# Kernel optimization log

Measured on AMD Instinct MI355X. Metric: run time of the kernel, lower is better.

Reference implementation:

```python
import jax, jax.numpy as jnp
import numpy as np

N_SAMPLES = 2 ** 15          # 32768
STEP = 256                   # transform_step_size
WIN = 2048                   # transform/synthesis window
N_FRAMES = N_SAMPLES // STEP # 128
N_COEFFS = WIN // 2 + 1      # 1025
DILATIONS = (1, 2, 4, 8, 16, 32, 64, 1)


def hann(n):
    return 0.5 - 0.5 * jnp.cos(2.0 * jnp.pi * jnp.arange(n, dtype=jnp.float32) / n)


def transform(audio):
    # audio: (B, 1, N) -> magnitude STFT (B, 1024, 128)
    x = audio[:, 0, :]
    x = jnp.pad(x, ((0, 0), (0, WIN - STEP)))  # pad so n_frames == N_SAMPLES // STEP
    idx = np.arange(N_FRAMES)[:, None] * STEP + np.arange(WIN)[None, :]
    frames = x[:, idx] * hann(WIN)
    spec = jnp.abs(jnp.fft.rfft(frames, norm='ortho'))   # (B, F, 1025)
    return spec[..., : N_COEFFS - 1].transpose(0, 2, 1)  # (B, 1024, F)


def conv1x1(x, w, b):
    # x: (B, I, T), w: (O, I, 1), b: (O,)
    return jnp.einsum('oi,bit->bot', w[:, :, 0], x) + b[None, :, None]


def anticausal_block(x, w, b, dilation):
    # kernel_size=2 anti-causal dilated conv: looks at t and t+dilation (pad future)
    x_fut = jnp.pad(x, ((0, 0), (0, 0), (0, dilation)))[:, :, dilation:]
    y = (jnp.einsum('oi,bit->bot', w[:, :, 0], x)
         + jnp.einsum('oi,bit->bot', w[:, :, 1], x_fut)
         + b[None, :, None])
    y = jax.nn.leaky_relu(y, 0.2)
    y = y + x
    # do_norm: per-example max-norm
    y = y / (jnp.max(jnp.abs(y), axis=(1, 2), keepdims=True) + 1e-8)
    return y


def upsample_with_holes(x, desired_size):
    # zero-stuffing upsample: out[..., ::step] = x
    b, c, t = x.shape
    step = desired_size // t
    out = jnp.zeros((b, c, desired_size), x.dtype)
    return out.at[:, :, ::step].set(x)


def freq_domain_resonance(coeffs):
    # coeffs: (1, C, 1025) in [0, 1); per-frame decay = repeated spectral multiply
    c = jnp.clip(coeffs, 0.0, 0.9999)
    exps = jnp.arange(1, N_FRAMES + 1, dtype=coeffs.dtype)
    mags = c[:, :, None, :] ** exps[None, None, :, None]     # (1, C, F, 1025)
    frames = jnp.fft.irfft(mags, n=WIN) * hann(WIN)
    hop = WIN // 2
    total = hop * (N_FRAMES - 1) + WIN
    idx = np.arange(N_FRAMES)[:, None] * hop + np.arange(WIN)[None, :]
    out = jnp.zeros(frames.shape[:2] + (total,), frames.dtype)
    out = out.at[:, :, idx].add(frames)                      # overlap-add
    return out[..., :N_SAMPLES]                              # (1, C, N)


def fft_convolve(a, b):
    # circular-free conv via zero-padding to 2N, keep first N (matches repo fft_convolve)
    n = a.shape[-1]
    spec = jnp.fft.rfft(a, n=2 * n) * jnp.fft.rfft(b, n=2 * n)
    return jnp.fft.irfft(spec, n=2 * n)[..., :n]


def reference(audio, proj_in_w, proj_in_b, blocks_w, blocks_b,
              proj_sparse_w, proj_sparse_b, proj_dense_w, proj_dense_b, resonances):
    spec = transform(audio)                         # (B, 1024, 128)
    h = conv1x1(spec, proj_in_w, proj_in_b)         # (B, 32, 128)
    acc = jnp.zeros_like(h)
    for i, d in enumerate(DILATIONS):               # fixed 8-block stack
        h = anticausal_block(h, blocks_w[i], blocks_b[i], d)
        acc = acc + h
    x = conv1x1(acc, proj_sparse_w, proj_sparse_b)  # (B, 256, 128)
    sparse = jax.nn.relu(x)
    x = conv1x1(sparse, proj_dense_w, proj_dense_b) # (B, 32, 128)
    x = upsample_with_holes(x, N_SAMPLES)           # (B, 32, 32768)
    res = freq_domain_resonance(resonances)         # (1, 32, 32768), broadcast over B
    y = fft_convolve(x, res)                        # (B, 32, 32768)
    y = jnp.sum(y, axis=1, keepdims=True)           # (B, 1, 32768)
    return y, sparse


def setup_inputs() -> dict:
    key = jax.random.key(0)
    ks = jax.random.split(key, 12)
    u = lambda k, shape: jax.random.uniform(k, shape, jnp.float32, -0.05, 0.05)
    return {
        'audio': jax.random.normal(ks[0], (32, 1, N_SAMPLES), jnp.float32),
        'proj_in_w': u(ks[1], (32, 1024, 1)),
        'proj_in_b': jnp.zeros((32,), jnp.float32),
        'blocks_w': u(ks[2], (8, 32, 32, 2)),
        'blocks_b': jnp.zeros((8, 32), jnp.float32),
        'proj_sparse_w': u(ks[3], (256, 32, 1)),
        'proj_sparse_b': jnp.zeros((256,), jnp.float32),
        'proj_dense_w': u(ks[4], (32, 256, 1)),
        'proj_dense_b': jnp.zeros((32,), jnp.float32),
        'resonances': jax.random.uniform(ks[5], (1, 32, N_COEFFS), jnp.float32, 0.0, 1.0),
    }
```

## Files before the change

### kernel.cpp

```cpp
#include <hip/hip_runtime.h>

#define PI_F 3.14159265358979323846f

typedef short bf16x8 __attribute__((ext_vector_type(8)));
typedef float f32x4 __attribute__((ext_vector_type(4)));

#define MFMA16(acc, a, b) \
  acc = __builtin_amdgcn_mfma_f32_16x16x32_bf16(a, b, acc, 0, 0, 0)

#define WS_SPEC   0u
#define WS_H0     4194304u
#define WS_ACC    4325376u
#define WS_V      4456448u
#define WS_WTIN   4587520u
#define WS_WST    4620288u
#define WS_WDT    4628480u
#define WS_FRAMES 4636672u
#define WS_RES    6733824u

__device__ __forceinline__ void fft2048_stages(float2* buf, int tid) {
  for (int stage = 0; stage < 11; ++stage) {
    int half = 1 << stage;
    float base = -PI_F / (float)half;
    for (int t = tid; t < 1024; t += 256) {
      int j  = t & (half - 1);
      int i0 = ((t >> stage) << (stage + 1)) + j;
      int i1 = i0 + half;
      float s, c;
      __sincosf(base * (float)j, &s, &c);
      float2 u = buf[i0];
      float2 w = buf[i1];
      float tr = c * w.x - s * w.y;
      float ti = c * w.y + s * w.x;
      buf[i0] = make_float2(u.x + tr, u.y + ti);
      buf[i1] = make_float2(u.x - tr, u.y - ti);
    }
    __syncthreads();
  }
}

__global__ __launch_bounds__(256) void k_fft(const float* __restrict__ audio,
                                             const float* __restrict__ resin,
                                             float* __restrict__ spec,
                                             float* __restrict__ frames) {
  __shared__ float2 buf[2048];
  int blk = blockIdx.x;
  if (blk < 2048) {
    int b  = blk >> 6;
    int f0 = (blk & 63) * 2;
    for (int j = threadIdx.x; j < 2048; j += 256) {
      float h = 0.5f - 0.5f * __cosf(0.0030679615757712823f * (float)j);
      int i1 = f0 * 256 + j;
      int i2 = i1 + 256;
      float a1 = (i1 < 32768) ? audio[b * 32768 + i1] : 0.f;
      float a2 = (i2 < 32768) ? audio[b * 32768 + i2] : 0.f;
      buf[__brev((unsigned)j) >> 21] = make_float2(a1 * h, a2 * h);
    }
    __syncthreads();
    fft2048_stages(buf, threadIdx.x);
    const float scale = 0.5f * 0.022097086912079608f;
    for (int k = threadIdx.x; k < 1024; k += 256) {
      float2 zk = buf[k];
      float2 zn = buf[(2048 - k) & 2047];
      float f1r = zk.x + zn.x, f1i = zk.y - zn.y;
      float f2r = zk.y + zn.y, f2i = zk.x - zn.x;
      spec[(b * 128 + f0) * 1024 + k]     = sqrtf(f1r * f1r + f1i * f1i) * scale;
      spec[(b * 128 + f0 + 1) * 1024 + k] = sqrtf(f2r * f2r + f2i * f2i) * scale;
    }
  } else {
    int r = blk - 2048;
    int c = r >> 4;
    int g = r & 15;
    float e1 = (float)(2 * g + 1);
    for (int k = threadIdx.x; k < 2048; k += 256) {
      int kk = (k <= 1024) ? k : 2048 - k;
      float cv = resin[c * 1025 + kk];
      cv = fminf(fmaxf(cv, 0.f), 0.9999f);
      float m1 = __powf(cv, e1);
      float m2 = m1 * cv;
      buf[__brev((unsigned)k) >> 21] = make_float2(m1, m2);
    }
    __syncthreads();
    fft2048_stages(buf, threadIdx.x);
    for (int j = threadIdx.x; j < 2048; j += 256) {
      float h  = 0.5f - 0.5f * __cosf(0.0030679615757712823f * (float)j);
      float sc = h * (1.f / 2048.f);
      float2 z = buf[j];
      frames[(c * 32 + 2 * g) * 2048 + j]     = z.x * sc;
      frames[(c * 32 + 2 * g + 1) * 2048 + j] = z.y * sc;
    }
  }
}

__global__ __launch_bounds__(256) void k_prep(const float* __restrict__ Win,
                                              const float* __restrict__ Ws,
                                              const float* __restrict__ Wd,
                                              const float* __restrict__ bwIn,
                                              float* __restrict__ WT,
                                              float* __restrict__ WsT,
                                              float* __restrict__ WdT,
                                              short* __restrict__ Whg,
                                              short* __restrict__ Wlg) {
  int i = blockIdx.x * 256 + threadIdx.x;
  if (i < 32768) { int o = i >> 10, k = i & 1023; WT[k * 32 + o] = Win[i]; }
  if (i < 8192)  { int o2 = i >> 5, m = i & 31;   WsT[m * 256 + o2] = Ws[i]; }
  if (i < 8192)  { int c = i >> 8, o2 = i & 255;  WdT[o2 * 32 + c] = Wd[i]; }
  if (i < 16384) {
    int w = i & 1, m = (i >> 1) & 31, o = (i >> 6) & 31, s = i >> 11;
    float val = bwIn[i];
    unsigned bits = __float_as_uint(val);
    float rem = val - __uint_as_float(bits & 0xffff0000u);
    int row = (s * 2 + w) * 32 + o;
    Whg[row * 32 + m] = (short)(bits >> 16);
    Wlg[row * 32 + m] = (short)(__float_as_uint(rem) >> 16);
  }
}

__global__ __launch_bounds__(256) void k_proj_in(const float* __restrict__ spec,
                                                 const float* __restrict__ WT,
                                                 const float* __restrict__ bias,
                                                 float* __restrict__ h0) {
  __shared__ float specL[8][1024];
  __shared__ float red[32][8][8];
  int b  = blockIdx.x >> 4;
  int t0 = (blockIdx.x & 15) * 8;
  for (int i = threadIdx.x; i < 8192; i += 256) {
    int tt = i >> 10, k = i & 1023;
    specL[tt][k] = spec[(b * 128 + t0 + tt) * 1024 + k];
  }
  __syncthreads();
  int o = threadIdx.x & 31, p = threadIdx.x >> 5;
  float part[8] = {0.f,0.f,0.f,0.f,0.f,0.f,0.f,0.f};
  for (int i = 0; i < 128; ++i) {
    int k = p * 128 + ((i + p * 4) & 127);
    float w = WT[k * 32 + o];
#pragma unroll
    for (int tt = 0; tt < 8; ++tt) part[tt] += w * specL[tt][k];
  }
#pragma unroll
  for (int tt = 0; tt < 8; ++tt) red[o][tt][p] = part[tt];
  __syncthreads();
  int oo = threadIdx.x >> 3, tt2 = threadIdx.x & 7;
  float s = bias[oo];
#pragma unroll
  for (int p2 = 0; p2 < 8; ++p2) s += red[oo][tt2][p2];
  h0[b * 4096 + oo * 128 + t0 + tt2] = s;
}

__global__ __launch_bounds__(1024) void k_chain(const float* __restrict__ h0,
                                                const short* __restrict__ Whg,
                                                const short* __restrict__ Wlg,
                                                const float* __restrict__ bb,
                                                float* __restrict__ accout) {
  __shared__ __align__(16) short Hh[192 * 40];
  __shared__ __align__(16) short Hl[192 * 40];
  __shared__ float Hf[128 * 33];
  __shared__ float bL[256];
  __shared__ float red[16];
  int b = blockIdx.x, tid = threadIdx.x;

  for (int i = tid; i < 4096; i += 1024) {
    int t = i & 127;
    int o = i >> 7;
    float val = h0[b * 4096 + i];
    Hf[t * 33 + o] = val;
    unsigned bits = __float_as_uint(val);
    float rem = val - __uint_as_float(bits & 0xffff0000u);
    Hh[t * 40 + o] = (short)(bits >> 16);
    Hl[t * 40 + o] = (short)(__float_as_uint(rem) >> 16);
  }
  for (int i = tid; i < 64 * 40; i += 1024) {
    Hh[128 * 40 + i] = 0;
    Hl[128 * 40 + i] = 0;
  }
  if (tid < 256) bL[tid] = bb[tid];
  __syncthreads();

  int wave = tid >> 6, lane = tid & 63;
  int quad = lane >> 4, l15 = lane & 15;
  int t0 = (wave & 7) * 16, o0 = (wave >> 3) * 16;
  int tD = t0 + quad * 4;
  int oD = o0 + l15;

  const bf16x8* Hh8 = (const bf16x8*)Hh;
  const bf16x8* Hl8 = (const bf16x8*)Hl;
  const bf16x8* Wh8 = (const bf16x8*)Whg;
  const bf16x8* Wl8 = (const bf16x8*)Wlg;

  float accsum[4] = {0.f, 0.f, 0.f, 0.f};
  const int DIL[8] = {1, 2, 4, 8, 16, 32, 64, 1};

#pragma unroll
  for (int s = 0; s < 8; ++s) {
    int arow = t0 + l15;
    int frow = arow + DIL[s];
    bf16x8 Ah = Hh8[arow * 5 + quad];
    bf16x8 Al = Hl8[arow * 5 + quad];
    bf16x8 Fh = Hh8[frow * 5 + quad];
    bf16x8 Fl = Hl8[frow * 5 + quad];
    int w0row = ((s * 2 + 0) * 32 + oD) * 4 + quad;
    int w1row = ((s * 2 + 1) * 32 + oD) * 4 + quad;
    bf16x8 B0h = Wh8[w0row], B0l = Wl8[w0row];
    bf16x8 B1h = Wh8[w1row], B1l = Wl8[w1row];
    float bias = bL[s * 32 + oD];
    f32x4 acc = {bias, bias, bias, bias};
    MFMA16(acc, Ah, B0h); MFMA16(acc, Ah, B0l); MFMA16(acc, Al, B0h);
    MFMA16(acc, Fh, B1h); MFMA16(acc, Fh, B1l); MFMA16(acc, Fl, B1h);
    float hnew[4], lmax = 0.f;
#pragma unroll
    for (int r = 0; r < 4; ++r) {
      float sv = acc[r];
      sv = (sv > 0.f) ? sv : 0.2f * sv;
      sv += Hf[(tD + r) * 33 + oD];
      hnew[r] = sv;
      lmax = fmaxf(lmax, fabsf(sv));
    }
#pragma unroll
    for (int off = 32; off > 0; off >>= 1)
      lmax = fmaxf(lmax, __shfl_down(lmax, off, 64));
    if (lane == 0) red[wave] = lmax;
    __syncthreads();
    float mx = red[0];
#pragma unroll
    for (int i = 1; i < 16; ++i) mx = fmaxf(mx, red[i]);
    float nm = 1.f / (mx + 1e-8f);
#pragma unroll
    for (int r = 0; r < 4; ++r) {
      float hv = hnew[r] * nm;
      accsum[r] += hv;
      int t = tD + r;
      Hf[t * 33 + oD] = hv;
      unsigned bits = __float_as_uint(hv);
      float rem = hv - __uint_as_float(bits & 0xffff0000u);
      Hh[t * 40 + oD] = (short)(bits >> 16);
      Hl[t * 40 + oD] = (short)(__float_as_uint(rem) >> 16);
    }
    __syncthreads();
  }
#pragma unroll
  for (int r = 0; r < 4; ++r)
    accout[b * 4096 + (tD + r) * 32 + oD] = accsum[r];
}

__global__ __launch_bounds__(256) void k_sparse_dense(const float* __restrict__ acc,
                                                      const float* __restrict__ WsT,
                                                      const float* __restrict__ bs,
                                                      const float* __restrict__ WdT,
                                                      const float* __restrict__ bd,
                                                      float* __restrict__ out_sparse,
                                                      float* __restrict__ v) {
  __shared__ float accL[32];
  __shared__ float sL[256];
  __shared__ float red[8][32];
  int b = blockIdx.x >> 7, t = blockIdx.x & 127;
  int tid = threadIdx.x;
  if (tid < 32) accL[tid] = acc[b * 4096 + t * 32 + tid];
  __syncthreads();
  float s = bs[tid];
  for (int m = 0; m < 32; ++m) s += WsT[m * 256 + tid] * accL[m];
  s = fmaxf(s, 0.f);
  out_sparse[b * 32768 + tid * 128 + t] = s;
  sL[tid] = s;
  __syncthreads();
  int c = tid & 31, p = tid >> 5;
  float part = 0.f;
  for (int j = 0; j < 32; ++j) {
    int o2 = p * 32 + j;
    part += WdT[o2 * 32 + c] * sL[o2];
  }
  red[p][c] = part;
  __syncthreads();
  if (tid < 32) {
    float vv = bd[tid];
    for (int p2 = 0; p2 < 8; ++p2) vv += red[p2][tid];
    v[b * 4096 + tid * 128 + t] = vv;
  }
}

__global__ __launch_bounds__(256) void k_res_assemble(const float* __restrict__ frames,
                                                      float* __restrict__ res) {
  int i = blockIdx.x * 256 + threadIdx.x;
  int c = i >> 15, s = i & 32767;
  int g = s >> 10, j0 = s & 1023;
  float v = frames[(c * 32 + g) * 2048 + j0];
  if (g > 0) v += frames[(c * 32 + g - 1) * 2048 + j0 + 1024];
  res[i] = v;
}

__global__ __launch_bounds__(256) void k_bpack(const float* __restrict__ res,
                                               short* __restrict__ Bh,
                                               short* __restrict__ Bl) {
  int c = blockIdx.x >> 4, o = blockIdx.x & 15;
  int r = threadIdx.x;
  bf16x8 hv, lv;
#pragma unroll
  for (int j = 0; j < 8; ++j) {
    float val = res[c * 32768 + (8 * o + j) * 256 + r];
    unsigned bits = __float_as_uint(val);
    float rem = val - __uint_as_float(bits & 0xffff0000u);
    hv[j] = (short)(bits >> 16);
    lv[j] = (short)(__float_as_uint(rem) >> 16);
  }
  int unit = (blockIdx.x * 16 + (r >> 4)) * 16 + (r & 15);
  ((bf16x8*)Bh)[unit] = hv;
  ((bf16x8*)Bl)[unit] = lv;
}

__global__ __launch_bounds__(256) void k_conv(const float* __restrict__ v,
                                              const short* __restrict__ Bh,
                                              const short* __restrict__ Bl,
                                              float* __restrict__ y) {
  __shared__ float vwin[32][33];
  __shared__ __align__(16) short Ah[16 * 520];
  __shared__ __align__(16) short Al[16 * 520];
  int blk = blockIdx.x;
  int b = blk / 36;
  int p = blk - b * 36;
  int qt = (int)((sqrtf(8.f * (float)p + 1.f) - 1.f) * 0.5f + 1e-4f);
  int uc = p - ((qt * (qt + 1)) >> 1);
  int q0 = qt * 16, u0 = uc * 16;
  int D0 = q0 - u0;

  for (int i = threadIdx.x; i < 1024; i += 256) {
    int c = i >> 5, ii = i & 31;
    int d = D0 - 15 + ii;
    vwin[c][ii] = (d >= 0 && d < 128) ? v[b * 4096 + c * 128 + d] : 0.f;
  }
  __syncthreads();
  for (int idx = threadIdx.x; idx < 8192; idx += 256) {
    int m = idx >> 9, kk = idx & 511;
    float val = vwin[kk >> 4][(m - (kk & 15)) + 15];
    unsigned bits = __float_as_uint(val);
    float rem = val - __uint_as_float(bits & 0xffff0000u);
    Ah[m * 520 + kk] = (short)(bits >> 16);
    Al[m * 520 + kk] = (short)(__float_as_uint(rem) >> 16);
  }
  __syncthreads();

  int lane = threadIdx.x & 63, wave = threadIdx.x >> 6;
  int quad = lane >> 4, l15 = lane & 15;
  int nt0 = wave * 4;

  f32x4 acc[4];
#pragma unroll
  for (int i = 0; i < 4; ++i) acc[i] = (f32x4)0.f;

  const bf16x8* Ah8 = (const bf16x8*)Ah;
  const bf16x8* Al8 = (const bf16x8*)Al;
  const bf16x8* Bh8 = (const bf16x8*)Bh;
  const bf16x8* Bl8 = (const bf16x8*)Bl;
  int aoff = l15 * 65 + quad;
  int og   = 2 * uc + (quad & 1);
  int cq   = quad >> 1;

#pragma unroll
  for (int ks = 0; ks < 16; ++ks) {
    bf16x8 avh = Ah8[aoff + 4 * ks];
    bf16x8 avl = Al8[aoff + 4 * ks];
    int c = 2 * ks + cq;
    int bbase = (c * 16 + og) * 256 + l15;
#pragma unroll
    for (int t = 0; t < 4; ++t) {
      int bi = bbase + (nt0 + t) * 16;
      bf16x8 bvh = Bh8[bi];
      bf16x8 bvl = Bl8[bi];
      MFMA16(acc[t], avh, bvh);
      MFMA16(acc[t], avh, bvl);
      MFMA16(acc[t], avl, bvh);
    }
  }

  float* yb = y + b * 32768 + (q0 + quad * 4) * 256 + l15;
#pragma unroll
  for (int t = 0; t < 4; ++t)
#pragma unroll
    for (int reg = 0; reg < 4; ++reg)
      atomicAdd(yb + reg * 256 + (nt0 + t) * 16, acc[t][reg]);
}

extern "C" void kernel_launch(void* const* d_in, const int* in_sizes, int n_in,
                              void* d_out, int out_size, void* d_ws, size_t ws_size,
                              hipStream_t stream) {
  const float* audio = (const float*)d_in[0];
  const float* Win   = (const float*)d_in[1];
  const float* bin   = (const float*)d_in[2];
  const float* bw    = (const float*)d_in[3];
  const float* bb    = (const float*)d_in[4];
  const float* Ws    = (const float*)d_in[5];
  const float* bs    = (const float*)d_in[6];
  const float* Wd    = (const float*)d_in[7];
  const float* bd    = (const float*)d_in[8];
  const float* reson = (const float*)d_in[9];

  float* out = (float*)d_out;
  float* ws  = (float*)d_ws;

  float* spec   = ws + WS_SPEC;
  float* h0     = ws + WS_H0;
  float* accb   = ws + WS_ACC;
  float* vbuf   = ws + WS_V;
  float* WT     = ws + WS_WTIN;
  float* WsT    = ws + WS_WST;
  float* WdT    = ws + WS_WDT;
  float* frames = ws + WS_FRAMES;
  float* resbuf = ws + WS_RES;
  short* Bh = (short*)(ws + WS_FRAMES);
  short* Bl = (short*)(ws + WS_FRAMES + 524288u);
  short* Whg = (short*)(ws + WS_V);
  short* Wlg = (short*)(ws + WS_V + 8192u);

  hipMemsetAsync(d_out, 0, 1048576u * sizeof(float), stream);

  k_prep<<<128, 256, 0, stream>>>(Win, Ws, Wd, bw, WT, WsT, WdT, Whg, Wlg);
  k_fft<<<2560, 256, 0, stream>>>(audio, reson, spec, frames);
  k_res_assemble<<<4096, 256, 0, stream>>>(frames, resbuf);
  k_bpack<<<512, 256, 0, stream>>>(resbuf, Bh, Bl);
  k_proj_in<<<512, 256, 0, stream>>>(spec, WT, bin, h0);
  k_chain<<<32, 1024, 0, stream>>>(h0, Whg, Wlg, bb, accb);
  k_sparse_dense<<<4096, 256, 0, stream>>>(accb, WsT, bs, WdT, bd, out + 1048576, vbuf);
  k_conv<<<1152, 256, 0, stream>>>(vbuf, Bh, Bl, out);
}
```

Baseline: 209.8 us.

## Prepack Toeplitz A operand globally and reuse B fragments across four output tiles

```diff
diff --git a/kernel.cpp b/kernel.cpp
--- a/kernel.cpp
+++ b/kernel.cpp
@@ -306,76 +306,85 @@
   ((bf16x8*)Bl)[unit] = lv;
 }
 
-__global__ __launch_bounds__(256) void k_conv(const float* __restrict__ v,
+__global__ __launch_bounds__(256) void k_apack(const float* __restrict__ v,
+                                               short* __restrict__ Ahx,
+                                               short* __restrict__ Alx) {
+  int row = blockIdx.x;
+  int b = row >> 7, mp = row & 127;
+  for (int kk = threadIdx.x; kk < 512; kk += 256) {
+    int c = kk >> 4, u = kk & 15, d = mp - u;
+    float val = (d >= 0) ? v[b * 4096 + c * 128 + d] : 0.f;
+    unsigned bits = __float_as_uint(val);
+    float rem = val - __uint_as_float(bits & 0xffff0000u);
+    Ahx[row * 512 + kk] = (short)(bits >> 16);
+    Alx[row * 512 + kk] = (short)(__float_as_uint(rem) >> 16);
+  }
+}
+
+__global__ __launch_bounds__(256) void k_conv(const short* __restrict__ Ahx,
+                                              const short* __restrict__ Alx,
                                               const short* __restrict__ Bh,
                                               const short* __restrict__ Bl,
                                               float* __restrict__ y) {
-  __shared__ float vwin[32][33];
-  __shared__ __align__(16) short Ah[16 * 520];
-  __shared__ __align__(16) short Al[16 * 520];
+  const int UC[12]  = {0,0,1,1,2,2,3,3,4,5,6,7};
+  const int QT0[12] = {0,4,1,5,2,6,3,7,4,5,6,7};
+  const int QN[12]  = {4,4,4,3,4,2,4,1,4,3,2,1};
   int blk = blockIdx.x;
-  int b = blk / 36;
-  int p = blk - b * 36;
-  int qt = (int)((sqrtf(8.f * (float)p + 1.f) - 1.f) * 0.5f + 1e-4f);
-  int uc = p - ((qt * (qt + 1)) >> 1);
-  int q0 = qt * 16, u0 = uc * 16;
-  int D0 = q0 - u0;
-
-  for (int i = threadIdx.x; i < 1024; i += 256) {
-    int c = i >> 5, ii = i & 31;
-    int d = D0 - 15 + ii;
-    vwin[c][ii] = (d >= 0 && d < 128) ? v[b * 4096 + c * 128 + d] : 0.f;
-  }
-  __syncthreads();
-  for (int idx = threadIdx.x; idx < 8192; idx += 256) {
-    int m = idx >> 9, kk = idx & 511;
-    float val = vwin[kk >> 4][(m - (kk & 15)) + 15];
-    unsigned bits = __float_as_uint(val);
-    float rem = val - __uint_as_float(bits & 0xffff0000u);
-    Ah[m * 520 + kk] = (short)(bits >> 16);
-    Al[m * 520 + kk] = (short)(__float_as_uint(rem) >> 16);
-  }
-  __syncthreads();
-
+  int b = blk / 12, g = blk - b * 12;
+  int uc = UC[g], qt0v = QT0[g], qn = QN[g];
   int lane = threadIdx.x & 63, wave = threadIdx.x >> 6;
   int quad = lane >> 4, l15 = lane & 15;
   int nt0 = wave * 4;
-
-  f32x4 acc[4];
-#pragma unroll
-  for (int i = 0; i < 4; ++i) acc[i] = (f32x4)0.f;
-
-  const bf16x8* Ah8 = (const bf16x8*)Ah;
-  const bf16x8* Al8 = (const bf16x8*)Al;
+  int og = 2 * uc + (quad & 1);
+  int cq = quad >> 1;
+
+  f32x4 acc[4][4];
+#pragma unroll
+  for (int j = 0; j < 4; ++j)
+#pragma unroll
+    for (int t = 0; t < 4; ++t) acc[j][t] = (f32x4)0.f;
+
+  const bf16x8* Ah8 = (const bf16x8*)Ahx;
+  const bf16x8* Al8 = (const bf16x8*)Alx;
   const bf16x8* Bh8 = (const bf16x8*)Bh;
   const bf16x8* Bl8 = (const bf16x8*)Bl;
-  int aoff = l15 * 65 + quad;
-  int og   = 2 * uc + (quad & 1);
-  int cq   = quad >> 1;
+  int abase0 = (b * 128 + (qt0v - uc) * 16 + l15) * 64 + quad;
 
 #pragma unroll
   for (int ks = 0; ks < 16; ++ks) {
-    bf16x8 avh = Ah8[aoff + 4 * ks];
-    bf16x8 avl = Al8[aoff + 4 * ks];
     int c = 2 * ks + cq;
     int bbase = (c * 16 + og) * 256 + l15;
+    bf16x8 bvh[4], bvl[4];
 #pragma unroll
     for (int t = 0; t < 4; ++t) {
       int bi = bbase + (nt0 + t) * 16;
-      bf16x8 bvh = Bh8[bi];
-      bf16x8 bvl = Bl8[bi];
-      MFMA16(acc[t], avh, bvh);
-      MFMA16(acc[t], avh, bvl);
-      MFMA16(acc[t], avl, bvh);
-    }
-  }
-
-  float* yb = y + b * 32768 + (q0 + quad * 4) * 256 + l15;
-#pragma unroll
-  for (int t = 0; t < 4; ++t)
-#pragma unroll
-    for (int reg = 0; reg < 4; ++reg)
-      atomicAdd(yb + reg * 256 + (nt0 + t) * 16, acc[t][reg]);
+      bvh[t] = Bh8[bi];
+      bvl[t] = Bl8[bi];
+    }
+#pragma unroll
+    for (int j = 0; j < 4; ++j) {
+      int ai = abase0 + j * 1024 + 4 * ks;
+      bf16x8 avh = Ah8[ai];
+      bf16x8 avl = Al8[ai];
+#pragma unroll
+      for (int t = 0; t < 4; ++t) {
+        MFMA16(acc[j][t], avh, bvh[t]);
+        MFMA16(acc[j][t], avh, bvl[t]);
+        MFMA16(acc[j][t], avl, bvh[t]);
+      }
+    }
+  }
+
+#pragma unroll
+  for (int j = 0; j < 4; ++j) {
+    if (j >= qn) break;
+    float* yb = y + b * 32768 + ((qt0v + j) * 16 + quad * 4) * 256 + l15;
+#pragma unroll
+    for (int t = 0; t < 4; ++t)
+#pragma unroll
+      for (int reg = 0; reg < 4; ++reg)
+        atomicAdd(yb + reg * 256 + (nt0 + t) * 16, acc[j][t][reg]);
+  }
 }
 
 extern "C" void kernel_launch(void* const* d_in, const int* in_sizes, int n_in,
@@ -408,6 +417,8 @@
   short* Bl = (short*)(ws + WS_FRAMES + 524288u);
   short* Whg = (short*)(ws + WS_V);
   short* Wlg = (short*)(ws + WS_V + 8192u);
+  short* Ahx = (short*)(ws + WS_SPEC);
+  short* Alx = (short*)(ws + WS_SPEC + 1048576u);
 
   hipMemsetAsync(d_out, 0, 1048576u * sizeof(float), stream);
 
@@ -418,5 +429,6 @@
   k_proj_in<<<512, 256, 0, stream>>>(spec, WT, bin, h0);
   k_chain<<<32, 1024, 0, stream>>>(h0, Whg, Wlg, bb, accb);
   k_sparse_dense<<<4096, 256, 0, stream>>>(accb, WsT, bs, WdT, bd, out + 1048576, vbuf);
-  k_conv<<<1152, 256, 0, stream>>>(vbuf, Bh, Bl, out);
-}
+  k_apack<<<4096, 256, 0, stream>>>(vbuf, Ahx, Alx);
+  k_conv<<<384, 256, 0, stream>>>(Ahx, Alx, Bh, Bl, out);
+}
```

Measured after the change: 225.0 us. 1.07x slower.

## Replace Toeplitz MFMA convolution with polyphase FFT convolution over frame index

Applied to the files above, without the earlier changes.

```diff
diff --git a/kernel.cpp b/kernel.cpp
--- a/kernel.cpp
+++ b/kernel.cpp
@@ -8,6 +8,11 @@
 #define MFMA16(acc, a, b) \
   acc = __builtin_amdgcn_mfma_f32_16x16x32_bf16(a, b, acc, 0, 0, 0)
 
+#define WS_RR     0u
+#define WS_RI     1056768u
+#define WS_VR     2113536u
+#define WS_VI     2245632u
+#define WS_YR     2377728u
 #define WS_SPEC   0u
 #define WS_H0     4194304u
 #define WS_ACC    4325376u
@@ -16,7 +21,7 @@
 #define WS_WST    4620288u
 #define WS_WDT    4628480u
 #define WS_FRAMES 4636672u
-#define WS_RES    6733824u
+#define WS_YI     4636672u
 
 __device__ __forceinline__ void fft2048_stages(float2* buf, int tid) {
   for (int stage = 0; stage < 11; ++stage) {
@@ -34,6 +39,29 @@
       float ti = c * w.y + s * w.x;
       buf[i0] = make_float2(u.x + tr, u.y + ti);
       buf[i1] = make_float2(u.x - tr, u.y - ti);
+    }
+    __syncthreads();
+  }
+}
+
+template<int NROWS>
+__device__ __forceinline__ void fft256_rows(float2 (*buf)[256], int tid, float sgn) {
+  for (int stage = 0; stage < 8; ++stage) {
+    int half = 1 << stage;
+    float base = sgn * PI_F / (float)half;
+    for (int t = tid; t < NROWS * 128; t += 256) {
+      int row = t >> 7, tt = t & 127;
+      int j  = tt & (half - 1);
+      int i0 = ((tt >> stage) << (stage + 1)) + j;
+      int i1 = i0 + half;
+      float s, c;
+      __sincosf(base * (float)j, &s, &c);
+      float2 u = buf[row][i0];
+      float2 w = buf[row][i1];
+      float tr = c * w.x - s * w.y;
+      float ti = c * w.y + s * w.x;
+      buf[row][i0] = make_float2(u.x + tr, u.y + ti);
+      buf[row][i1] = make_float2(u.x - tr, u.y - ti);
     }
     __syncthreads();
   }
@@ -277,105 +305,113 @@
   }
 }
 
-__global__ __launch_bounds__(256) void k_res_assemble(const float* __restrict__ frames,
-                                                      float* __restrict__ res) {
-  int i = blockIdx.x * 256 + threadIdx.x;
-  int c = i >> 15, s = i & 32767;
-  int g = s >> 10, j0 = s & 1023;
-  float v = frames[(c * 32 + g) * 2048 + j0];
-  if (g > 0) v += frames[(c * 32 + g - 1) * 2048 + j0 + 1024];
-  res[i] = v;
-}
-
-__global__ __launch_bounds__(256) void k_bpack(const float* __restrict__ res,
-                                               short* __restrict__ Bh,
-                                               short* __restrict__ Bl) {
-  int c = blockIdx.x >> 4, o = blockIdx.x & 15;
-  int r = threadIdx.x;
-  bf16x8 hv, lv;
-#pragma unroll
-  for (int j = 0; j < 8; ++j) {
-    float val = res[c * 32768 + (8 * o + j) * 256 + r];
-    unsigned bits = __float_as_uint(val);
-    float rem = val - __uint_as_float(bits & 0xffff0000u);
-    hv[j] = (short)(bits >> 16);
-    lv[j] = (short)(__float_as_uint(rem) >> 16);
-  }
-  int unit = (blockIdx.x * 16 + (r >> 4)) * 16 + (r & 15);
-  ((bf16x8*)Bh)[unit] = hv;
-  ((bf16x8*)Bl)[unit] = lv;
-}
-
-__global__ __launch_bounds__(256) void k_conv(const float* __restrict__ v,
-                                              const short* __restrict__ Bh,
-                                              const short* __restrict__ Bl,
-                                              float* __restrict__ y) {
-  __shared__ float vwin[32][33];
-  __shared__ __align__(16) short Ah[16 * 520];
-  __shared__ __align__(16) short Al[16 * 520];
-  int blk = blockIdx.x;
-  int b = blk / 36;
-  int p = blk - b * 36;
-  int qt = (int)((sqrtf(8.f * (float)p + 1.f) - 1.f) * 0.5f + 1e-4f);
-  int uc = p - ((qt * (qt + 1)) >> 1);
-  int q0 = qt * 16, u0 = uc * 16;
-  int D0 = q0 - u0;
-
-  for (int i = threadIdx.x; i < 1024; i += 256) {
-    int c = i >> 5, ii = i & 31;
-    int d = D0 - 15 + ii;
-    vwin[c][ii] = (d >= 0 && d < 128) ? v[b * 4096 + c * 128 + d] : 0.f;
-  }
-  __syncthreads();
-  for (int idx = threadIdx.x; idx < 8192; idx += 256) {
-    int m = idx >> 9, kk = idx & 511;
-    float val = vwin[kk >> 4][(m - (kk & 15)) + 15];
-    unsigned bits = __float_as_uint(val);
-    float rem = val - __uint_as_float(bits & 0xffff0000u);
-    Ah[m * 520 + kk] = (short)(bits >> 16);
-    Al[m * 520 + kk] = (short)(__float_as_uint(rem) >> 16);
-  }
-  __syncthreads();
-
-  int lane = threadIdx.x & 63, wave = threadIdx.x >> 6;
-  int quad = lane >> 4, l15 = lane & 15;
-  int nt0 = wave * 4;
-
-  f32x4 acc[4];
-#pragma unroll
-  for (int i = 0; i < 4; ++i) acc[i] = (f32x4)0.f;
-
-  const bf16x8* Ah8 = (const bf16x8*)Ah;
-  const bf16x8* Al8 = (const bf16x8*)Al;
-  const bf16x8* Bh8 = (const bf16x8*)Bh;
-  const bf16x8* Bl8 = (const bf16x8*)Bl;
-  int aoff = l15 * 65 + quad;
-  int og   = 2 * uc + (quad & 1);
-  int cq   = quad >> 1;
-
-#pragma unroll
-  for (int ks = 0; ks < 16; ++ks) {
-    bf16x8 avh = Ah8[aoff + 4 * ks];
-    bf16x8 avl = Al8[aoff + 4 * ks];
-    int c = 2 * ks + cq;
-    int bbase = (c * 16 + og) * 256 + l15;
-#pragma unroll
-    for (int t = 0; t < 4; ++t) {
-      int bi = bbase + (nt0 + t) * 16;
-      bf16x8 bvh = Bh8[bi];
-      bf16x8 bvl = Bl8[bi];
-      MFMA16(acc[t], avh, bvh);
-      MFMA16(acc[t], avh, bvl);
-      MFMA16(acc[t], avl, bvh);
-    }
-  }
-
-  float* yb = y + b * 32768 + (q0 + quad * 4) * 256 + l15;
-#pragma unroll
-  for (int t = 0; t < 4; ++t)
-#pragma unroll
-    for (int reg = 0; reg < 4; ++reg)
-      atomicAdd(yb + reg * 256 + (nt0 + t) * 16, acc[t][reg]);
+__global__ __launch_bounds__(256) void k_rfft(const float* __restrict__ frames,
+                                              float* __restrict__ Rr,
+                                              float* __restrict__ Ri) {
+  __shared__ float2 buf[32][256];
+  int c = blockIdx.x >> 3, rg = blockIdx.x & 7;
+  for (int t = threadIdx.x; t < 4096; t += 256) {
+    int u = t >> 5, rr = t & 31;
+    int s = u * 256 + rg * 32 + rr;
+    int g = s >> 10, j0 = s & 1023;
+    float val = frames[(c * 32 + g) * 2048 + j0];
+    if (g > 0) val += frames[(c * 32 + g - 1) * 2048 + j0 + 1024];
+    int bi = __brev((unsigned)u) >> 24;
+    buf[rr][bi]     = make_float2(val, 0.f);
+    buf[rr][bi | 1] = make_float2(0.f, 0.f);
+  }
+  __syncthreads();
+  fft256_rows<32>(buf, threadIdx.x, -1.f);
+  for (int t = threadIdx.x; t < 129 * 32; t += 256) {
+    int k = t >> 5, rr = t & 31;
+    int idx = (k * 32 + c) * 256 + rg * 32 + rr;
+    Rr[idx] = buf[rr][k].x;
+    Ri[idx] = buf[rr][k].y;
+  }
+}
+
+__global__ __launch_bounds__(256) void k_vfft(const float* __restrict__ v,
+                                              float* __restrict__ Vr,
+                                              float* __restrict__ Vi) {
+  __shared__ float2 buf[16][256];
+  int b = blockIdx.x >> 1, ch = blockIdx.x & 1;
+  for (int t = threadIdx.x; t < 2048; t += 256) {
+    int c2 = t >> 7, u = t & 127;
+    float val = v[b * 4096 + (ch * 16 + c2) * 128 + u];
+    int bi = __brev((unsigned)u) >> 24;
+    buf[c2][bi]     = make_float2(val, 0.f);
+    buf[c2][bi | 1] = make_float2(0.f, 0.f);
+  }
+  __syncthreads();
+  fft256_rows<16>(buf, threadIdx.x, -1.f);
+  for (int t = threadIdx.x; t < 129 * 16; t += 256) {
+    int k = t >> 4, c2 = t & 15;
+    int idx = (k * 32 + b) * 32 + ch * 16 + c2;
+    Vr[idx] = buf[c2][k].x;
+    Vi[idx] = buf[c2][k].y;
+  }
+}
+
+__global__ __launch_bounds__(256) void k_cgemm(const float* __restrict__ Vr,
+                                               const float* __restrict__ Vi,
+                                               const float* __restrict__ Rr,
+                                               const float* __restrict__ Ri,
+                                               float* __restrict__ Yr,
+                                               float* __restrict__ Yi) {
+  __shared__ float2 Vs[32][32];
+  int k = blockIdx.x >> 1, rh = blockIdx.x & 1;
+  for (int t = threadIdx.x; t < 1024; t += 256)
+    Vs[t >> 5][t & 31] = make_float2(Vr[k * 1024 + t], Vi[k * 1024 + t]);
+  __syncthreads();
+  int r = rh * 128 + (threadIdx.x & 127);
+  int half = threadIdx.x >> 7;
+  float yre[16], yim[16];
+#pragma unroll
+  for (int i = 0; i < 16; ++i) { yre[i] = 0.f; yim[i] = 0.f; }
+  for (int c = 0; c < 32; ++c) {
+    float rrv = Rr[(k * 32 + c) * 256 + r];
+    float riv = Ri[(k * 32 + c) * 256 + r];
+#pragma unroll
+    for (int bbv = 0; bbv < 16; ++bbv) {
+      float2 vc = Vs[half * 16 + bbv][c];
+      yre[bbv] += vc.x * rrv - vc.y * riv;
+      yim[bbv] += vc.x * riv + vc.y * rrv;
+    }
+  }
+#pragma unroll
+  for (int bbv = 0; bbv < 16; ++bbv) {
+    int b = half * 16 + bbv;
+    Yr[(k * 32 + b) * 256 + r] = yre[bbv];
+    Yi[(k * 32 + b) * 256 + r] = yim[bbv];
+  }
+}
+
+__global__ __launch_bounds__(256) void k_yifft(const float* __restrict__ Yr,
+                                               const float* __restrict__ Yi,
+                                               float* __restrict__ y) {
+  __shared__ float2 buf[32][256];
+  int b = blockIdx.x >> 3, rg = blockIdx.x & 7;
+  int r0 = rg * 32;
+  for (int t = threadIdx.x; t < 8192; t += 256) {
+    int k = t >> 5, rr = t & 31;
+    float re, im;
+    if (k <= 128) {
+      re = Yr[(k * 32 + b) * 256 + r0 + rr];
+      im = Yi[(k * 32 + b) * 256 + r0 + rr];
+    } else {
+      int kk = 256 - k;
+      re =  Yr[(kk * 32 + b) * 256 + r0 + rr];
+      im = -Yi[(kk * 32 + b) * 256 + r0 + rr];
+    }
+    buf[rr][__brev((unsigned)k) >> 24] = make_float2(re, im);
+  }
+  __syncthreads();
+  fft256_rows<32>(buf, threadIdx.x, 1.f);
+  const float inv = 1.f / 256.f;
+  for (int t = threadIdx.x; t < 4096; t += 256) {
+    int q = t >> 5, rr = t & 31;
+    y[b * 32768 + q * 256 + r0 + rr] = buf[rr][q].x * inv;
+  }
 }
 
 extern "C" void kernel_launch(void* const* d_in, const int* in_sizes, int n_in,
@@ -403,20 +439,22 @@
   float* WsT    = ws + WS_WST;
   float* WdT    = ws + WS_WDT;
   float* frames = ws + WS_FRAMES;
-  float* resbuf = ws + WS_RES;
-  short* Bh = (short*)(ws + WS_FRAMES);
-  short* Bl = (short*)(ws + WS_FRAMES + 524288u);
   short* Whg = (short*)(ws + WS_V);
   short* Wlg = (short*)(ws + WS_V + 8192u);
-
-  hipMemsetAsync(d_out, 0, 1048576u * sizeof(float), stream);
+  float* Rr = ws + WS_RR;
+  float* Ri = ws + WS_RI;
+  float* Vr = ws + WS_VR;
+  float* Vi = ws + WS_VI;
+  float* Yr = ws + WS_YR;
+  float* Yi = ws + WS_YI;
 
   k_prep<<<128, 256, 0, stream>>>(Win, Ws, Wd, bw, WT, WsT, WdT, Whg, Wlg);
   k_fft<<<2560, 256, 0, stream>>>(audio, reson, spec, frames);
-  k_res_assemble<<<4096, 256, 0, stream>>>(frames, resbuf);
-  k_bpack<<<512, 256, 0, stream>>>(resbuf, Bh, Bl);
   k_proj_in<<<512, 256, 0, stream>>>(spec, WT, bin, h0);
+  k_rfft<<<256, 256, 0, stream>>>(frames, Rr, Ri);
   k_chain<<<32, 1024, 0, stream>>>(h0, Whg, Wlg, bb, accb);
   k_sparse_dense<<<4096, 256, 0, stream>>>(accb, WsT, bs, WdT, bd, out + 1048576, vbuf);
-  k_conv<<<1152, 256, 0, stream>>>(vbuf, Bh, Bl, out);
-}
+  k_vfft<<<64, 256, 0, stream>>>(vbuf, Vr, Vi);
+  k_cgemm<<<258, 256, 0, stream>>>(Vr, Vi, Rr, Ri, Yr, Yi);
+  k_yifft<<<256, 256, 0, stream>>>(Yr, Yi, out);
+}
```

Result: slower. 239.5 us (+14.2%).
